# Kernel optimization log

Hardware: AMD Instinct MI355X
Metric: run time of the kernel (lower is better)

## Reference

```python
import jax, jax.numpy as jnp
import numpy as np

N = 50000       # nodes
E = 800000      # edges (avg degree 16)
DIN = 128
DOUT = 128
ALPHA = 0.2     # leaky relu negative slope


def setup_inputs() -> dict:
    key = jax.random.key(0)
    k1, k2, k3, k4, k5 = jax.random.split(key, 5)
    h = jax.random.normal(k1, (N, DIN), dtype=jnp.float32)
    # xavier-normal-ish scaling for params
    W = jax.random.normal(k2, (DIN, DOUT), dtype=jnp.float32) * np.float32(np.sqrt(2.0 / (DIN + DOUT)))
    a = jax.random.normal(k3, (2 * DOUT,), dtype=jnp.float32) * np.float32(np.sqrt(2.0 / (2 * DOUT + 1)))
    src = jax.random.randint(k4, (E,), 0, N, dtype=jnp.int32)
    dst = jax.random.randint(k5, (E,), 0, N, dtype=jnp.int32)
    return {"h": h, "W": W, "a": a, "src": src, "dst": dst}


def reference(h, W, a, src, dst):
    # eval mode: dropout is a no-op (training=False)
    Wh = h @ W                                  # [N, DOUT]
    a_src, a_dst = a[:DOUT], a[DOUT:]
    s = Wh @ a_src                              # [N] per-node src score
    d = Wh @ a_dst                              # [N] per-node dst score
    e = jax.nn.leaky_relu(s[src] + d[dst], negative_slope=ALPHA)  # [E]
    # segment softmax over incoming edges of each dst node
    emax = jax.ops.segment_max(e, dst, num_segments=N)            # [N]
    emax = jnp.where(jnp.isfinite(emax), emax, jnp.float32(0.0))  # isolated nodes
    ex = jnp.exp(e - emax[dst])                                   # [E]
    denom = jax.ops.segment_sum(ex, dst, num_segments=N)          # [N]
    alpha = ex / denom[dst]                                       # [E]
    # weighted scatter-sum of src features into dst nodes
    h_out = jax.ops.segment_sum(alpha[:, None] * Wh[src], dst, num_segments=N)  # [N, DOUT]
    # residual: in_feats == out_feats -> Identity
    return h_out + h
```

## Files before the change

### kernel.cpp

```cpp
#include <hip/hip_runtime.h>
#include <math.h>

#define NN 50000
#define NE 800000
#define DD 128
#define LRELU 0.2f
#define CAP 64
#define SLICE 6256

typedef unsigned int uint;
typedef unsigned short ushort;
using short8 = __attribute__((ext_vector_type(8))) short;
using f32x4  = __attribute__((ext_vector_type(4))) float;

__device__ __forceinline__ uint pack_bf2(float x, float y) {
  uint a = __float_as_uint(x), b = __float_as_uint(y);
  a = (a + 0x7fffu + ((a >> 16) & 1u)) >> 16;
  b = (b + 0x7fffu + ((b >> 16) & 1u)) >> 16;
  return a | (b << 16);
}
__device__ __forceinline__ ushort pack_bf1(float x) {
  uint a = __float_as_uint(x);
  return (ushort)((a + 0x7fffu + ((a >> 16) & 1u)) >> 16);
}

__global__ __launch_bounds__(256) void k_prep(const float* __restrict__ W,
                                              const float* __restrict__ a,
                                              float* __restrict__ wsv,
                                              float* __restrict__ wdv,
                                              ushort* __restrict__ Wtg) {
  const int tid = threadIdx.x;
  int idx = blockIdx.x * 256 + tid;
  int c = idx >> 7, k = idx & 127;
  Wtg[idx] = pack_bf1(W[k * DD + c]);

  if (blockIdx.x == 0 && tid < DD) {
    float accs = 0.f, accd = 0.f;
    for (int cc = 0; cc < DD; ++cc) {
      float w = W[tid * DD + cc];
      accs = fmaf(w, a[cc], accs);
      accd = fmaf(w, a[DD + cc], accd);
    }
    wsv[tid] = accs;
    wdv[tid] = accd;
  }
}

__global__ __launch_bounds__(256) void k_gemm2(const float* __restrict__ h,
                                               const float* __restrict__ wsv,
                                               const float* __restrict__ wdv,
                                               const ushort* __restrict__ Wtg,
                                               float* __restrict__ sv,
                                               float* __restrict__ dv,
                                               uint* __restrict__ Whb,
                                               int* __restrict__ cnt) {
  __shared__ ushort WtS[16384];
  __shared__ ushort hbs[8192];
  __shared__ float stage[4][16][18];
  const int tid = threadIdx.x;

  if (tid < 64) {
    int idx = blockIdx.x * 64 + tid;
    if (idx < NN) cnt[idx] = 0;
  }

#pragma unroll
  for (int it = 0; it < 16; ++it) {
    int chunk = it * 256 + tid;
    int c = chunk >> 4, kc = chunk & 15;
    short8 v = *reinterpret_cast<const short8*>(Wtg + chunk * 8);
    *reinterpret_cast<short8*>(
        reinterpret_cast<char*>(WtS) + c * 256 + ((kc ^ (c & 7)) << 4)) = v;
  }

  const int wave = tid >> 6, l = tid & 63;
  const int cg = l & 15;
  const int c8 = cg * 8;
  float4 w0 = *reinterpret_cast<const float4*>(wsv + c8);
  float4 w1 = *reinterpret_cast<const float4*>(wsv + c8 + 4);
  float4 d0 = *reinterpret_cast<const float4*>(wdv + c8);
  float4 d1 = *reinterpret_cast<const float4*>(wdv + c8 + 4);
#pragma unroll
  for (int rr = 0; rr < 4; ++rr) {
    int row = wave * 16 + rr * 4 + (l >> 4);
    int grow = blockIdx.x * 64 + row;
    int gsrc = grow < NN ? grow : 0;
    float4 h0 = *reinterpret_cast<const float4*>(h + (size_t)gsrc * DD + c8);
    float4 h1 = *reinterpret_cast<const float4*>(h + (size_t)gsrc * DD + c8 + 4);
    float ps = h0.x*w0.x + h0.y*w0.y + h0.z*w0.z + h0.w*w0.w
             + h1.x*w1.x + h1.y*w1.y + h1.z*w1.z + h1.w*w1.w;
    float pd = h0.x*d0.x + h0.y*d0.y + h0.z*d0.z + h0.w*d0.w
             + h1.x*d1.x + h1.y*d1.y + h1.z*d1.z + h1.w*d1.w;
#pragma unroll
    for (int off = 1; off < 16; off <<= 1) {
      ps += __shfl_xor(ps, off);
      pd += __shfl_xor(pd, off);
    }
    if (cg == 0 && grow < NN) { sv[grow] = ps; dv[grow] = pd; }
    uint4 u;
    u.x = pack_bf2(h0.x, h0.y); u.y = pack_bf2(h0.z, h0.w);
    u.z = pack_bf2(h1.x, h1.y); u.w = pack_bf2(h1.z, h1.w);
    *reinterpret_cast<uint4*>(
        reinterpret_cast<char*>(hbs) + row * 256 + ((cg ^ (row & 7)) << 4)) = u;
  }
  __syncthreads();

  const int lane = l;
  const int arow16 = lane & 15;
  const int garow = blockIdx.x * 64 + wave * 16 + arow16;
  const bool rok = garow < NN;

  short8 afr[4];
#pragma unroll
  for (int kg = 0; kg < 4; ++kg) {
    int row = wave * 16 + arow16;
    int g = kg * 4 + (lane >> 4);
    afr[kg] = *reinterpret_cast<const short8*>(
        reinterpret_cast<const char*>(hbs) + row * 256 + ((g ^ (row & 7)) << 4));
  }

  const int xb = lane & 7;
  for (int cb = 0; cb < 8; ++cb) {
    const int col = cb * 16 + (lane & 15);
    f32x4 acc = {0.f, 0.f, 0.f, 0.f};
#pragma unroll
    for (int kg = 0; kg < 4; ++kg) {
      int kchunk = kg * 4 + (lane >> 4);
      short8 bfr = *reinterpret_cast<const short8*>(
          reinterpret_cast<const char*>(WtS) + col * 256 + ((kchunk ^ xb) << 4));
      acc = __builtin_amdgcn_mfma_f32_16x16x32_bf16(afr[kg], bfr, acc, 0, 0, 0);
    }
    float (*st)[18] = stage[wave];
#pragma unroll
    for (int j = 0; j < 4; ++j) st[(lane >> 4) * 4 + j][lane & 15] = acc[j];
    __asm__ volatile("s_waitcnt lgkmcnt(0)" ::: "memory");
    __builtin_amdgcn_sched_barrier(0);
    if (rok) {
#pragma unroll
      for (int j2 = 0; j2 < 2; ++j2) {
        int p = (lane >> 4) + 4 * j2;
        float2 v = *reinterpret_cast<const float2*>(&st[lane & 15][2 * p]);
        Whb[(size_t)garow * 64 + cb * 8 + p] = pack_bf2(v.x, v.y);
      }
    }
    __asm__ volatile("s_waitcnt lgkmcnt(0)" ::: "memory");
    __builtin_amdgcn_sched_barrier(0);
  }
}

__global__ __launch_bounds__(256) void k_fill(const int* __restrict__ src,
                                              const int* __restrict__ dst,
                                              const float* __restrict__ sv,
                                              const float* __restrict__ dv,
                                              int* __restrict__ cnt,
                                              uint* __restrict__ entries) {
  const int xcd = blockIdx.x & 7;
  const int base = xcd * SLICE;
  const int e0 = (blockIdx.x >> 3) * 3125;
  const int e1 = e0 + 3125;
  for (int i = e0 + threadIdx.x; i < e1; i += 256) {
    int d = dst[i];
    if ((uint)(d - base) >= (uint)SLICE) continue;
    int s = src[i];
    float ev = sv[s] + dv[d];
    ev = ev > 0.f ? ev : LRELU * ev;
    float x = __expf(ev);
    int p = atomicAdd(&cnt[d], 1);
    if (p < CAP)
      atomicExch(&entries[(size_t)d * CAP + p],
                 ((uint)pack_bf1(x) << 16) | (uint)s);
  }
}

__global__ __launch_bounds__(256) void k_node(const float* __restrict__ h,
                                              const uint* __restrict__ Whb,
                                              const int* __restrict__ cnt,
                                              const uint* __restrict__ entries,
                                              float* __restrict__ out) {
  const int sl = blockIdx.x & 7;
  int wid = sl * SLICE + (blockIdx.x >> 3) * 4 + (threadIdx.x >> 6);
  const int lim = min(NN, (sl + 1) * SLICE);
  if (wid >= lim) return;
  wid = __builtin_amdgcn_readfirstlane(wid);
  const int lane = threadIdx.x & 63;

  float2 hrow = reinterpret_cast<const float2*>(h + (size_t)wid * DD)[lane];
  int deg = cnt[wid];
  deg = deg < CAP ? deg : CAP;
  float2* o2 = reinterpret_cast<float2*>(out + (size_t)wid * DD);
  if (deg == 0) { o2[lane] = hrow; return; }

  const uint* bucket = entries + (size_t)wid * CAP;
  const uint4* b4 = reinterpret_cast<const uint4*>(bucket);
  float2 ac0 = {0.f,0.f}, ac1 = {0.f,0.f}, ac2 = {0.f,0.f}, ac3 = {0.f,0.f};
  float den = 0.f;
  const int nq = deg >> 2;
  for (int q = 0; q < nq; ++q) {
    uint4 e4 = b4[q];
    float x0 = __uint_as_float(e4.x & 0xffff0000u);
    float x1 = __uint_as_float(e4.y & 0xffff0000u);
    float x2 = __uint_as_float(e4.z & 0xffff0000u);
    float x3 = __uint_as_float(e4.w & 0xffff0000u);
    uint u0 = Whb[(size_t)(e4.x & 0xffffu) * 64 + lane];
    uint u1 = Whb[(size_t)(e4.y & 0xffffu) * 64 + lane];
    uint u2 = Whb[(size_t)(e4.z & 0xffffu) * 64 + lane];
    uint u3 = Whb[(size_t)(e4.w & 0xffffu) * 64 + lane];
    den += (x0 + x1) + (x2 + x3);
    ac0.x = fmaf(x0, __uint_as_float(u0 << 16), ac0.x);
    ac0.y = fmaf(x0, __uint_as_float(u0 & 0xffff0000u), ac0.y);
    ac1.x = fmaf(x1, __uint_as_float(u1 << 16), ac1.x);
    ac1.y = fmaf(x1, __uint_as_float(u1 & 0xffff0000u), ac1.y);
    ac2.x = fmaf(x2, __uint_as_float(u2 << 16), ac2.x);
    ac2.y = fmaf(x2, __uint_as_float(u2 & 0xffff0000u), ac2.y);
    ac3.x = fmaf(x3, __uint_as_float(u3 << 16), ac3.x);
    ac3.y = fmaf(x3, __uint_as_float(u3 & 0xffff0000u), ac3.y);
  }
  for (int k = nq * 4; k < deg; ++k) {
    uint e = bucket[k];
    float x0 = __uint_as_float(e & 0xffff0000u);
    uint u0 = Whb[(size_t)(e & 0xffffu) * 64 + lane];
    den += x0;
    ac0.x = fmaf(x0, __uint_as_float(u0 << 16), ac0.x);
    ac0.y = fmaf(x0, __uint_as_float(u0 & 0xffff0000u), ac0.y);
  }
  float inv = 1.0f / den;
  float ax = (ac0.x + ac1.x) + (ac2.x + ac3.x);
  float ay = (ac0.y + ac1.y) + (ac2.y + ac3.y);
  o2[lane] = make_float2(hrow.x + ax * inv, hrow.y + ay * inv);
}

extern "C" void kernel_launch(void* const* d_in, const int* in_sizes, int n_in,
                              void* d_out, int out_size, void* d_ws, size_t ws_size,
                              hipStream_t stream) {
  const float* h = (const float*)d_in[0];
  const float* W = (const float*)d_in[1];
  const float* a = (const float*)d_in[2];
  const int* src = (const int*)d_in[3];
  const int* dst = (const int*)d_in[4];
  float* out = (float*)d_out;

  char* ws = (char*)d_ws;
  uint*   Whb     = (uint*)  (ws);
  uint*   entries = (uint*)  (ws + 12800000);
  ushort* Wtg     = (ushort*)(ws + 25600000);
  float*  sv      = (float*) (ws + 25632768);
  float*  dv      = (float*) (ws + 25832768);
  float*  wsv     = (float*) (ws + 26032768);
  float*  wdv     = (float*) (ws + 26033280);
  int*    cnt     = (int*)   (ws + 26033792);

  hipLaunchKernelGGL(k_prep, dim3(64), dim3(256), 0, stream, W, a, wsv, wdv, Wtg);
  hipLaunchKernelGGL(k_gemm2, dim3(782), dim3(256), 0, stream,
                     h, wsv, wdv, Wtg, sv, dv, Whb, cnt);
  hipLaunchKernelGGL(k_fill, dim3(2048), dim3(256), 0, stream,
                     src, dst, sv, dv, cnt, entries);
  hipLaunchKernelGGL(k_node, dim3(8 * (SLICE / 4)), dim3(256), 0, stream,
                     h, Whb, cnt, entries, out);
}
```

Baseline: 198.5 us.

## Replace per-node atomic bucket fill with two-pass counting sort into 64-node bins

Drops the fixed-capacity per-destination buckets filled with global atomics. Edges are now bucketed by a histogram, a scan and a binning pass into contiguous 64-node bins, with a local shared-memory sort per block. k_node then loads each bin into LDS, builds a CSR per node and aggregates neighbours, which removes the per-edge global atomics and the scattered 64-slot bucket reads. The cost is extra kernel launches, a single-block scan, and a BINCAP limit of 1280 edges per bin that silently drops edges if a bin overflows.

```diff
diff --git a/kernel.cpp b/kernel.cpp
--- a/kernel.cpp
+++ b/kernel.cpp
@@ -5,8 +5,10 @@
 #define NE 800000
 #define DD 128
 #define LRELU 0.2f
-#define CAP 64
-#define SLICE 6256
+#define NPB 64
+#define NB 782
+#define EPB 3125
+#define BINCAP 1280
 
 typedef unsigned int uint;
 typedef unsigned short ushort;
@@ -28,11 +30,13 @@
                                               const float* __restrict__ a,
                                               float* __restrict__ wsv,
                                               float* __restrict__ wdv,
-                                              ushort* __restrict__ Wtg) {
+                                              ushort* __restrict__ Wtg,
+                                              int* __restrict__ gcnt) {
   const int tid = threadIdx.x;
   int idx = blockIdx.x * 256 + tid;
   int c = idx >> 7, k = idx & 127;
   Wtg[idx] = pack_bf1(W[k * DD + c]);
+  if (idx < NB * 16) gcnt[idx] = 0;
 
   if (blockIdx.x == 0 && tid < DD) {
     float accs = 0.f, accd = 0.f;
@@ -52,17 +56,11 @@
                                                const ushort* __restrict__ Wtg,
                                                float* __restrict__ sv,
                                                float* __restrict__ dv,
-                                               uint* __restrict__ Whb,
-                                               int* __restrict__ cnt) {
+                                               uint* __restrict__ Whb) {
   __shared__ ushort WtS[16384];
   __shared__ ushort hbs[8192];
   __shared__ float stage[4][16][18];
   const int tid = threadIdx.x;
-
-  if (tid < 64) {
-    int idx = blockIdx.x * 64 + tid;
-    if (idx < NN) cnt[idx] = 0;
-  }
 
 #pragma unroll
   for (int it = 0; it < 16; ++it) {
@@ -148,85 +146,199 @@
   }
 }
 
-__global__ __launch_bounds__(256) void k_fill(const int* __restrict__ src,
-                                              const int* __restrict__ dst,
-                                              const float* __restrict__ sv,
-                                              const float* __restrict__ dv,
-                                              int* __restrict__ cnt,
-                                              uint* __restrict__ entries) {
-  const int xcd = blockIdx.x & 7;
-  const int base = xcd * SLICE;
-  const int e0 = (blockIdx.x >> 3) * 3125;
-  const int e1 = e0 + 3125;
-  for (int i = e0 + threadIdx.x; i < e1; i += 256) {
-    int d = dst[i];
-    if ((uint)(d - base) >= (uint)SLICE) continue;
-    int s = src[i];
+__global__ __launch_bounds__(256) void k_hist(const int* __restrict__ dst,
+                                              int* __restrict__ gcnt) {
+  __shared__ int lh[NB];
+  const int tid = threadIdx.x;
+  for (int i = tid; i < NB; i += 256) lh[i] = 0;
+  __syncthreads();
+  const int e0 = blockIdx.x * EPB;
+  for (int i = e0 + tid; i < e0 + EPB; i += 256)
+    atomicAdd(&lh[dst[i] >> 6], 1);
+  __syncthreads();
+  for (int i = tid; i < NB; i += 256)
+    if (lh[i]) atomicAdd(&gcnt[i * 16], lh[i]);
+}
+
+__global__ __launch_bounds__(256) void k_scan(const int* __restrict__ gcnt,
+                                              int* __restrict__ base,
+                                              int* __restrict__ cursor) {
+  __shared__ int part[256];
+  const int tid = threadIdx.x;
+  int v[4];
+#pragma unroll
+  for (int q = 0; q < 4; ++q) {
+    int idx = 4 * tid + q;
+    v[q] = idx < NB ? gcnt[idx * 16] : 0;
+  }
+  part[tid] = v[0] + v[1] + v[2] + v[3];
+  __syncthreads();
+  for (int off = 1; off < 256; off <<= 1) {
+    int a = part[tid];
+    int b = tid >= off ? part[tid - off] : 0;
+    __syncthreads();
+    part[tid] = a + b;
+    __syncthreads();
+  }
+  int run = tid ? part[tid - 1] : 0;
+#pragma unroll
+  for (int q = 0; q < 4; ++q) {
+    int idx = 4 * tid + q;
+    if (idx < NB) { base[idx] = run; cursor[idx * 16] = run; }
+    run += v[q];
+  }
+  if (tid == 255) base[NB] = part[255];
+}
+
+__global__ __launch_bounds__(256) void k_pass2(const int* __restrict__ src,
+                                               const int* __restrict__ dst,
+                                               const float* __restrict__ sv,
+                                               const float* __restrict__ dv,
+                                               int* __restrict__ cursor,
+                                               uint2* __restrict__ binbuf) {
+  __shared__ int lcnt[NB];
+  __shared__ int lofs[NB];
+  __shared__ int gbase[NB];
+  __shared__ int part[256];
+  __shared__ uint2 recs[EPB + 11];
+  __shared__ ushort binof[EPB + 11];
+  const int tid = threadIdx.x;
+  const int e0 = blockIdx.x * EPB;
+
+  for (int i = tid; i < NB; i += 256) lcnt[i] = 0;
+  __syncthreads();
+  for (int i = e0 + tid; i < e0 + EPB; i += 256)
+    atomicAdd(&lcnt[dst[i] >> 6], 1);
+  __syncthreads();
+  int v[4];
+#pragma unroll
+  for (int q = 0; q < 4; ++q) {
+    int idx = 4 * tid + q;
+    v[q] = idx < NB ? lcnt[idx] : 0;
+  }
+  part[tid] = v[0] + v[1] + v[2] + v[3];
+  __syncthreads();
+  for (int off = 1; off < 256; off <<= 1) {
+    int a = part[tid];
+    int b = tid >= off ? part[tid - off] : 0;
+    __syncthreads();
+    part[tid] = a + b;
+    __syncthreads();
+  }
+  int run = tid ? part[tid - 1] : 0;
+#pragma unroll
+  for (int q = 0; q < 4; ++q) {
+    int idx = 4 * tid + q;
+    if (idx < NB) {
+      lofs[idx] = run;
+      gbase[idx] = v[q] ? atomicAdd(&cursor[idx * 16], v[q]) : 0;
+    }
+    run += v[q];
+  }
+  __syncthreads();
+  for (int i = tid; i < NB; i += 256) lcnt[i] = lofs[i];
+  __syncthreads();
+  for (int i = e0 + tid; i < e0 + EPB; i += 256) {
+    int d = dst[i], s = src[i];
     float ev = sv[s] + dv[d];
     ev = ev > 0.f ? ev : LRELU * ev;
-    float x = __expf(ev);
-    int p = atomicAdd(&cnt[d], 1);
-    if (p < CAP)
-      atomicExch(&entries[(size_t)d * CAP + p],
-                 ((uint)pack_bf1(x) << 16) | (uint)s);
+    uint entry = ((uint)pack_bf1(__expf(ev)) << 16) | (uint)s;
+    int bin = d >> 6;
+    int p = atomicAdd(&lcnt[bin], 1);
+    recs[p] = make_uint2((uint)(d & 63), entry);
+    binof[p] = (ushort)bin;
+  }
+  __syncthreads();
+  for (int j = tid; j < EPB; j += 256) {
+    int b = binof[j];
+    binbuf[gbase[b] + (j - lofs[b])] = recs[j];
   }
 }
 
 __global__ __launch_bounds__(256) void k_node(const float* __restrict__ h,
                                               const uint* __restrict__ Whb,
-                                              const int* __restrict__ cnt,
-                                              const uint* __restrict__ entries,
+                                              const int* __restrict__ base,
+                                              const uint2* __restrict__ binbuf,
                                               float* __restrict__ out) {
-  const int sl = blockIdx.x & 7;
-  int wid = sl * SLICE + (blockIdx.x >> 3) * 4 + (threadIdx.x >> 6);
-  const int lim = min(NN, (sl + 1) * SLICE);
-  if (wid >= lim) return;
-  wid = __builtin_amdgcn_readfirstlane(wid);
-  const int lane = threadIdx.x & 63;
-
-  float2 hrow = reinterpret_cast<const float2*>(h + (size_t)wid * DD)[lane];
-  int deg = cnt[wid];
-  deg = deg < CAP ? deg : CAP;
-  float2* o2 = reinterpret_cast<float2*>(out + (size_t)wid * DD);
-  if (deg == 0) { o2[lane] = hrow; return; }
-
-  const uint* bucket = entries + (size_t)wid * CAP;
-  const uint4* b4 = reinterpret_cast<const uint4*>(bucket);
-  float2 ac0 = {0.f,0.f}, ac1 = {0.f,0.f}, ac2 = {0.f,0.f}, ac3 = {0.f,0.f};
-  float den = 0.f;
-  const int nq = deg >> 2;
-  for (int q = 0; q < nq; ++q) {
-    uint4 e4 = b4[q];
-    float x0 = __uint_as_float(e4.x & 0xffff0000u);
-    float x1 = __uint_as_float(e4.y & 0xffff0000u);
-    float x2 = __uint_as_float(e4.z & 0xffff0000u);
-    float x3 = __uint_as_float(e4.w & 0xffff0000u);
-    uint u0 = Whb[(size_t)(e4.x & 0xffffu) * 64 + lane];
-    uint u1 = Whb[(size_t)(e4.y & 0xffffu) * 64 + lane];
-    uint u2 = Whb[(size_t)(e4.z & 0xffffu) * 64 + lane];
-    uint u3 = Whb[(size_t)(e4.w & 0xffffu) * 64 + lane];
-    den += (x0 + x1) + (x2 + x3);
-    ac0.x = fmaf(x0, __uint_as_float(u0 << 16), ac0.x);
-    ac0.y = fmaf(x0, __uint_as_float(u0 & 0xffff0000u), ac0.y);
-    ac1.x = fmaf(x1, __uint_as_float(u1 << 16), ac1.x);
-    ac1.y = fmaf(x1, __uint_as_float(u1 & 0xffff0000u), ac1.y);
-    ac2.x = fmaf(x2, __uint_as_float(u2 << 16), ac2.x);
-    ac2.y = fmaf(x2, __uint_as_float(u2 & 0xffff0000u), ac2.y);
-    ac3.x = fmaf(x3, __uint_as_float(u3 << 16), ac3.x);
-    ac3.y = fmaf(x3, __uint_as_float(u3 & 0xffff0000u), ac3.y);
-  }
-  for (int k = nq * 4; k < deg; ++k) {
-    uint e = bucket[k];
-    float x0 = __uint_as_float(e & 0xffff0000u);
-    uint u0 = Whb[(size_t)(e & 0xffffu) * 64 + lane];
-    den += x0;
-    ac0.x = fmaf(x0, __uint_as_float(u0 << 16), ac0.x);
-    ac0.y = fmaf(x0, __uint_as_float(u0 & 0xffff0000u), ac0.y);
-  }
-  float inv = 1.0f / den;
-  float ax = (ac0.x + ac1.x) + (ac2.x + ac3.x);
-  float ay = (ac0.y + ac1.y) + (ac2.y + ac3.y);
-  o2[lane] = make_float2(hrow.x + ax * inv, hrow.y + ay * inv);
+  __shared__ uint2 ent[BINCAP];
+  __shared__ uint csr[BINCAP];
+  __shared__ int hist[NPB];
+  __shared__ int ofs[NPB + 1];
+  const int tid = threadIdx.x;
+  const int bin = blockIdx.x;
+  const int b0 = base[bin];
+  const int n = min(base[bin + 1] - b0, BINCAP);
+
+  for (int i = tid; i < n; i += 256) ent[i] = binbuf[b0 + i];
+  if (tid < NPB) hist[tid] = 0;
+  __syncthreads();
+  for (int i = tid; i < n; i += 256) atomicAdd(&hist[ent[i].x], 1);
+  __syncthreads();
+  if (tid < NPB) {
+    int val = hist[tid];
+    int inc = val;
+#pragma unroll
+    for (int off = 1; off < 64; off <<= 1) {
+      int t = __shfl_up(inc, off, 64);
+      if ((tid & 63) >= off) inc += t;
+    }
+    ofs[tid + 1] = inc;
+    if (tid == 0) ofs[0] = 0;
+    hist[tid] = inc - val;
+  }
+  __syncthreads();
+  for (int i = tid; i < n; i += 256) {
+    int d = ent[i].x;
+    int p = atomicAdd(&hist[d], 1);
+    csr[p] = ent[i].y;
+  }
+  __syncthreads();
+
+  const int wave = tid >> 6, lane = tid & 63;
+  for (int r = 0; r < NPB / 4; ++r) {
+    int nd = r * 4 + wave;
+    int gn = bin * NPB + nd;
+    if (gn >= NN) continue;
+    float2 hrow = reinterpret_cast<const float2*>(h + (size_t)gn * DD)[lane];
+    float2* o2 = reinterpret_cast<float2*>(out + (size_t)gn * DD);
+    int kb = ofs[nd], ke = ofs[nd + 1];
+    if (kb == ke) { o2[lane] = hrow; continue; }
+    float2 ac0 = {0.f,0.f}, ac1 = {0.f,0.f}, ac2 = {0.f,0.f}, ac3 = {0.f,0.f};
+    float den = 0.f;
+    int k = kb;
+    for (; k + 4 <= ke; k += 4) {
+      uint e0 = csr[k], e1 = csr[k+1], e2 = csr[k+2], e3 = csr[k+3];
+      float x0 = __uint_as_float(e0 & 0xffff0000u);
+      float x1 = __uint_as_float(e1 & 0xffff0000u);
+      float x2 = __uint_as_float(e2 & 0xffff0000u);
+      float x3 = __uint_as_float(e3 & 0xffff0000u);
+      uint u0 = Whb[(size_t)(e0 & 0xffffu) * 64 + lane];
+      uint u1 = Whb[(size_t)(e1 & 0xffffu) * 64 + lane];
+      uint u2 = Whb[(size_t)(e2 & 0xffffu) * 64 + lane];
+      uint u3 = Whb[(size_t)(e3 & 0xffffu) * 64 + lane];
+      den += (x0 + x1) + (x2 + x3);
+      ac0.x = fmaf(x0, __uint_as_float(u0 << 16), ac0.x);
+      ac0.y = fmaf(x0, __uint_as_float(u0 & 0xffff0000u), ac0.y);
+      ac1.x = fmaf(x1, __uint_as_float(u1 << 16), ac1.x);
+      ac1.y = fmaf(x1, __uint_as_float(u1 & 0xffff0000u), ac1.y);
+      ac2.x = fmaf(x2, __uint_as_float(u2 << 16), ac2.x);
+      ac2.y = fmaf(x2, __uint_as_float(u2 & 0xffff0000u), ac2.y);
+      ac3.x = fmaf(x3, __uint_as_float(u3 << 16), ac3.x);
+      ac3.y = fmaf(x3, __uint_as_float(u3 & 0xffff0000u), ac3.y);
+    }
+    for (; k < ke; ++k) {
+      uint e = csr[k];
+      float x0 = __uint_as_float(e & 0xffff0000u);
+      uint u0 = Whb[(size_t)(e & 0xffffu) * 64 + lane];
+      den += x0;
+      ac0.x = fmaf(x0, __uint_as_float(u0 << 16), ac0.x);
+      ac0.y = fmaf(x0, __uint_as_float(u0 & 0xffff0000u), ac0.y);
+    }
+    float inv = 1.0f / den;
+    float ax = (ac0.x + ac1.x) + (ac2.x + ac3.x);
+    float ay = (ac0.y + ac1.y) + (ac2.y + ac3.y);
+    o2[lane] = make_float2(hrow.x + ax * inv, hrow.y + ay * inv);
+  }
 }
 
 extern "C" void kernel_launch(void* const* d_in, const int* in_sizes, int n_in,
@@ -240,20 +352,24 @@
   float* out = (float*)d_out;
 
   char* ws = (char*)d_ws;
-  uint*   Whb     = (uint*)  (ws);
-  uint*   entries = (uint*)  (ws + 12800000);
-  ushort* Wtg     = (ushort*)(ws + 25600000);
-  float*  sv      = (float*) (ws + 25632768);
-  float*  dv      = (float*) (ws + 25832768);
-  float*  wsv     = (float*) (ws + 26032768);
-  float*  wdv     = (float*) (ws + 26033280);
-  int*    cnt     = (int*)   (ws + 26033792);
-
-  hipLaunchKernelGGL(k_prep, dim3(64), dim3(256), 0, stream, W, a, wsv, wdv, Wtg);
+  uint*   Whb    = (uint*)  (ws);
+  uint2*  binbuf = (uint2*) (ws + 12800000);
+  ushort* Wtg    = (ushort*)(ws + 19200000);
+  float*  sv     = (float*) (ws + 19232768);
+  float*  dv     = (float*) (ws + 19432768);
+  float*  wsv    = (float*) (ws + 19632768);
+  float*  wdv    = (float*) (ws + 19633280);
+  int*    gcnt   = (int*)   (ws + 19633792);
+  int*    cursor = (int*)   (ws + 19683840);
+  int*    base   = (int*)   (ws + 19733888);
+
+  hipLaunchKernelGGL(k_prep, dim3(64), dim3(256), 0, stream, W, a, wsv, wdv, Wtg, gcnt);
   hipLaunchKernelGGL(k_gemm2, dim3(782), dim3(256), 0, stream,
-                     h, wsv, wdv, Wtg, sv, dv, Whb, cnt);
-  hipLaunchKernelGGL(k_fill, dim3(2048), dim3(256), 0, stream,
-                     src, dst, sv, dv, cnt, entries);
-  hipLaunchKernelGGL(k_node, dim3(8 * (SLICE / 4)), dim3(256), 0, stream,
-                     h, Whb, cnt, entries, out);
-}
+                     h, wsv, wdv, Wtg, sv, dv, Whb);
+  hipLaunchKernelGGL(k_hist, dim3(256), dim3(256), 0, stream, dst, gcnt);
+  hipLaunchKernelGGL(k_scan, dim3(1), dim3(256), 0, stream, gcnt, base, cursor);
+  hipLaunchKernelGGL(k_pass2, dim3(256), dim3(256), 0, stream,
+                     src, dst, sv, dv, cursor, binbuf);
+  hipLaunchKernelGGL(k_node, dim3(NB), dim3(256), 0, stream,
+                     h, Whb, base, binbuf, out);
+}
```

Measured after the change: 187.4 us. -5.6%, faster.
